# Performance work log

Hardware: AMD Instinct MI355X
Metric: run time of the kernel (lower is better)

## Reference

```python
import jax, jax.numpy as jnp
import numpy as np

SEQ, B, IN, H = 512, 64, 1024, 1024

def _lstm_layer(x_seq, Wx, bx, Wh, bh):
    # x_seq: [S, B, D], Wx: [4H, D], Wh: [4H, H]
    h0 = jnp.zeros((x_seq.shape[1], Wh.shape[1]), x_seq.dtype)
    c0 = jnp.zeros_like(h0)
    def step(carry, x_t):
        h, c = carry
        z = x_t @ Wx.T + bx + h @ Wh.T + bh  # [B, 4H]
        i, f, g, o = jnp.split(z, 4, axis=1)
        c1 = jax.nn.sigmoid(f) * c + jax.nn.sigmoid(i) * jnp.tanh(g)
        h1 = jax.nn.sigmoid(o) * jnp.tanh(c1)
        return (h1, c1), h1
    _, hs = jax.lax.scan(step, (h0, c0), x_seq)
    return hs  # [S, B, H]

def setup_inputs() -> dict:
    key = jax.random.key(0)
    ks = jax.random.split(key, 9)
    s_in = 1.0 / np.sqrt(IN)
    s_h = 1.0 / np.sqrt(H)
    return {
        "x": jax.random.normal(ks[0], (SEQ, B, IN), jnp.float32),
        "Wx0": jax.random.uniform(ks[1], (4 * H, IN), jnp.float32, -s_in, s_in),
        "bx0": jax.random.uniform(ks[2], (4 * H,), jnp.float32, -s_in, s_in),
        "Wh0": jax.random.uniform(ks[3], (4 * H, H), jnp.float32, -s_h, s_h),
        "bh0": jax.random.uniform(ks[4], (4 * H,), jnp.float32, -s_h, s_h),
        "Wx1": jax.random.uniform(ks[5], (4 * H, H), jnp.float32, -s_h, s_h),
        "bx1": jax.random.uniform(ks[6], (4 * H,), jnp.float32, -s_h, s_h),
        "Wh1": jax.random.uniform(ks[7], (4 * H, H), jnp.float32, -s_h, s_h),
        "bh1": jax.random.uniform(ks[8], (4 * H,), jnp.float32, -s_h, s_h),
    }

def reference(x, Wx0, bx0, Wh0, bh0, Wx1, bx1, Wh1, bh1):
    # Two stacked unidirectional LSTM layers, zero initial states.
    h_seq0 = _lstm_layer(x, Wx0, bx0, Wh0, bh0)
    h_seq1 = _lstm_layer(h_seq0, Wx1, bx1, Wh1, bh1)
    return h_seq1  # [S, B, H] = stacked version of the torch list output
```

## Files before the change

kernel.cpp:

```cpp
#include <hip/hip_runtime.h>


#define SEQ   512
#define BATCH 64
#define HID   1024
#define NG    4096
#define KCAT  2048
#define EPOCH_IDX 8192

typedef __attribute__((ext_vector_type(8))) _Float16 f16x8;
typedef __attribute__((ext_vector_type(4))) _Float16 f16x4;
typedef __attribute__((ext_vector_type(4))) float    f32x4;

__device__ __forceinline__ float sigm_f(float x){ return 1.f/(1.f + __expf(-x)); }
__device__ __forceinline__ float tanh_f(float x){
    float e = __expf(-2.f*fabsf(x));
    float r = (1.f - e)/(1.f + e);
    return copysignf(r, x);
}

__device__ __forceinline__ void store_h8(_Float16* p, f16x4 v){
    asm volatile("global_store_dwordx2 %0, %1, off sc0 sc1" :: "v"(p), "v"(v) : "memory");
}
__device__ __forceinline__ void drain_vmem(){
    asm volatile("s_waitcnt vmcnt(0)" ::: "memory");
}


__global__ void prep_w_kernel(const float* __restrict__ Wx, const float* __restrict__ Wh,
                              const float* __restrict__ bx, const float* __restrict__ bh,
                              _Float16* __restrict__ Wr, float* __restrict__ br){
    int p = blockIdx.x;
    int j = p >> 2, g = p & 3;
    int r = g*1024 + j;
    int k = threadIdx.x * 8;
    const float* s = (k < 1024) ? (Wx + (size_t)r*1024 + k)
                                : (Wh + (size_t)r*1024 + (k - 1024));
    float4 v0 = *reinterpret_cast<const float4*>(s);
    float4 v1 = *reinterpret_cast<const float4*>(s + 4);
    f16x8 o;
    o[0]=(_Float16)v0.x; o[1]=(_Float16)v0.y; o[2]=(_Float16)v0.z; o[3]=(_Float16)v0.w;
    o[4]=(_Float16)v1.x; o[5]=(_Float16)v1.y; o[6]=(_Float16)v1.z; o[7]=(_Float16)v1.w;
    *reinterpret_cast<f16x8*>(Wr + (size_t)p*KCAT + k) = o;
    if (threadIdx.x == 0) br[p] = bx[r] + bh[r];
}

__global__ void prep_x_kernel(const float* __restrict__ x, _Float16* xo){
    size_t i = ((size_t)blockIdx.x*256 + threadIdx.x) * 8;
    float4 v0 = *reinterpret_cast<const float4*>(x + i);
    float4 v1 = *reinterpret_cast<const float4*>(x + i + 4);
    f16x8 o;
    o[0]=(_Float16)v0.x; o[1]=(_Float16)v0.y; o[2]=(_Float16)v0.z; o[3]=(_Float16)v0.w;
    o[4]=(_Float16)v1.x; o[5]=(_Float16)v1.y; o[6]=(_Float16)v1.z; o[7]=(_Float16)v1.w;
    *reinterpret_cast<f16x8*>(xo + i) = o;
}

__global__ void init_misc_kernel(int* flags, _Float16* hz){
    int i = blockIdx.x*256 + threadIdx.x;
    flags[i] = 0;
    size_t j = (size_t)i * 4;
    if (j < (size_t)BATCH*HID){
        f16x4 z; z[0]=(_Float16)0.f; z[1]=(_Float16)0.f; z[2]=(_Float16)0.f; z[3]=(_Float16)0.f;
        *reinterpret_cast<f16x4*>(hz + j) = z;
    }
}


__device__ __forceinline__ void wait_epoch_g(const int* flags, int k, int rep){
    for(;;){
        int e = __hip_atomic_load(&flags[EPOCH_IDX + rep*32], __ATOMIC_RELAXED, __HIP_MEMORY_SCOPE_AGENT);
        if (e >= k) break;
        __builtin_amdgcn_s_sleep(2);
    }
    asm volatile("" ::: "memory");
}

__device__ __forceinline__ void aggregate_publish(int* flags, int k, int lane){
    const int b = lane*4;
    for(;;){
        int a0 = __hip_atomic_load(&flags[(b+0)*32], __ATOMIC_RELAXED, __HIP_MEMORY_SCOPE_AGENT);
        int a1 = __hip_atomic_load(&flags[(b+1)*32], __ATOMIC_RELAXED, __HIP_MEMORY_SCOPE_AGENT);
        int a2 = __hip_atomic_load(&flags[(b+2)*32], __ATOMIC_RELAXED, __HIP_MEMORY_SCOPE_AGENT);
        int a3 = __hip_atomic_load(&flags[(b+3)*32], __ATOMIC_RELAXED, __HIP_MEMORY_SCOPE_AGENT);
        bool ok = (a0>=k) && (a1>=k) && (a2>=k) && (a3>=k);
        if (__all(ok)) break;
        __builtin_amdgcn_s_sleep(1);
    }
    asm volatile("" ::: "memory");
    if (lane < 8)
        __hip_atomic_store(&flags[EPOCH_IDX + lane*32], k, __ATOMIC_RELAXED, __HIP_MEMORY_SCOPE_AGENT);
}

__device__ __forceinline__ void lds_publish(int* e, int k){
    __hip_atomic_store(e, k, __ATOMIC_RELAXED, __HIP_MEMORY_SCOPE_WORKGROUP);
}
__device__ __forceinline__ void lds_wait(int* e, int k){
    while (__hip_atomic_load(e, __ATOMIC_RELAXED, __HIP_MEMORY_SCOPE_WORKGROUP) < k)
        __builtin_amdgcn_s_sleep(1);
    asm volatile("" ::: "memory");
}


__device__ __forceinline__ f32x4 mfma16(f16x8 a, f16x8 b, f32x4 c){
    return __builtin_amdgcn_mfma_f32_16x16x32_f16(a, b, c, 0, 0, 0);
}

__device__ __forceinline__ void gemm_q_f16(const _Float16* A, const _Float16* Wp, f32x4* acc){
    #pragma unroll 4
    for (int kk = 0; kk < 16; ++kk){
        f16x8 b  = *reinterpret_cast<const f16x8*>(Wp + kk*32);
        f16x8 a0 = *reinterpret_cast<const f16x8*>(A + kk*32);
        f16x8 a1 = *reinterpret_cast<const f16x8*>(A + kk*32 + 16*1024);
        f16x8 a2 = *reinterpret_cast<const f16x8*>(A + kk*32 + 32*1024);
        f16x8 a3 = *reinterpret_cast<const f16x8*>(A + kk*32 + 48*1024);
        acc[0] = mfma16(a0, b, acc[0]);
        acc[1] = mfma16(a1, b, acc[1]);
        acc[2] = mfma16(a2, b, acc[2]);
        acc[3] = mfma16(a3, b, acc[3]);
    }
}

__device__ __forceinline__ void gemm_q_f32(const float* A, const _Float16* Wp, f32x4* acc){
    #pragma unroll 2
    for (int kk = 0; kk < 16; ++kk){
        f16x8 b = *reinterpret_cast<const f16x8*>(Wp + kk*32);
        f16x8 a[4];
        #pragma unroll
        for (int m = 0; m < 4; ++m){
            float4 u0 = *reinterpret_cast<const float4*>(A + kk*32 + (size_t)m*16*1024);
            float4 u1 = *reinterpret_cast<const float4*>(A + kk*32 + (size_t)m*16*1024 + 4);
            f16x8 v;
            v[0]=(_Float16)u0.x; v[1]=(_Float16)u0.y; v[2]=(_Float16)u0.z; v[3]=(_Float16)u0.w;
            v[4]=(_Float16)u1.x; v[5]=(_Float16)u1.y; v[6]=(_Float16)u1.z; v[7]=(_Float16)u1.w;
            a[m] = v;
        }
        acc[0] = mfma16(a[0], b, acc[0]);
        acc[1] = mfma16(a[1], b, acc[1]);
        acc[2] = mfma16(a[2], b, acc[2]);
        acc[3] = mfma16(a[3], b, acc[3]);
    }
}


__global__ __launch_bounds__(256, 1)
void lstm_persist(const _Float16* __restrict__ Wr0, const _Float16* __restrict__ Wr1,
                  const float* __restrict__ br0, const float* __restrict__ br1,
                  const _Float16* __restrict__ xbf, const float* __restrict__ xf32,
                  int use_xf16, const _Float16* __restrict__ hz,
                  _Float16* h0ring, _Float16* h1ring, float* out, int* flags){
    const int tid  = threadIdx.x;
    const int wg   = blockIdx.x;
    const int wv   = tid >> 6;
    const int lane = tid & 63;
    const int r    = lane & 15;
    const int q    = lane >> 4;
    const int p0   = wg * 16;
    const int rep  = wg & 7;

    __shared__ float accL[2][4][64][17];
    __shared__ int   lds_epoch;

    if (tid == 0) lds_epoch = 0;
    __syncthreads();

    f32x4 cst = {0.f,0.f,0.f,0.f};
    f32x4 ho_keep = {0.f,0.f,0.f,0.f};
    f32x4 bias[4];
    {
        const float* bsrc = (wv == 0) ? br0 : br1;
        #pragma unroll
        for (int jj = 0; jj < 4; ++jj)
            bias[jj] = *reinterpret_cast<const f32x4*>(&bsrc[p0 + jj*4]);
    }

    const int kofs = (wv & 1)*512 + q*8;
    const int wcol = wv*512 + q*8;

    for (int k = 0; k <= SEQ; ++k){
        f32x4 acc0[4], acc1[4];
        #pragma unroll
        for (int m = 0; m < 4; ++m){
            acc0[m].x=0;acc0[m].y=0;acc0[m].z=0;acc0[m].w=0;
            acc1[m].x=0;acc1[m].y=0;acc1[m].z=0;acc1[m].w=0;
        }

        if (wv < 2){
            if (k < SEQ){
                if (use_xf16)
                    gemm_q_f16(xbf + (size_t)k*BATCH*HID + (size_t)r*HID + kofs,
                               Wr0 + (size_t)(p0 + r)*KCAT + wcol, acc0);
                else
                    gemm_q_f32(xf32 + (size_t)k*BATCH*1024 + (size_t)r*1024 + kofs,
                               Wr0 + (size_t)(p0 + r)*KCAT + wcol, acc0);
            }
            if (k > 0){
                lds_wait(&lds_epoch, k);
                gemm_q_f16(h0ring + (size_t)(k-1)*BATCH*HID + (size_t)r*HID + kofs,
                           Wr1 + (size_t)(p0 + r)*KCAT + wcol, acc1);
            }
        } else {
            if (k > 0){
                if (wv == 3){
                    if (wg == 0) aggregate_publish(flags, k, lane);
                    else         wait_epoch_g(flags, k, rep);
                    lds_publish(&lds_epoch, k);
                } else {
                    lds_wait(&lds_epoch, k);
                }
            }
            if (k < SEQ){
                const _Float16* A0 = (k == 0) ? (hz + (size_t)r*HID + kofs)
                                              : (h0ring + (size_t)(k-1)*BATCH*HID + (size_t)r*HID + kofs);
                gemm_q_f16(A0, Wr0 + (size_t)(p0 + r)*KCAT + wcol, acc0);
            }
            if (k >= 1){
                const _Float16* A1 = (k == 1) ? (hz + (size_t)r*HID + kofs)
                                              : (h1ring + (size_t)(k-2)*BATCH*HID + (size_t)r*HID + kofs);
                gemm_q_f16(A1, Wr1 + (size_t)(p0 + r)*KCAT + wcol, acc1);
            }
        }

        __syncthreads();

        #pragma unroll
        for (int mt = 0; mt < 4; ++mt){
            #pragma unroll
            for (int j = 0; j < 4; ++j){
                accL[0][wv][mt*16 + q*4 + j][r] = acc0[mt][j];
                accL[1][wv][mt*16 + q*4 + j][r] = acc1[mt][j];
            }
        }
        __syncthreads();

        if (wv == 0 && k < SEQ){
            f32x4 zz[4];
            #pragma unroll
            for (int jj = 0; jj < 4; ++jj) zz[jj] = bias[jj];
            #pragma unroll
            for (int w2 = 0; w2 < 4; ++w2)
                #pragma unroll
                for (int jj = 0; jj < 4; ++jj){
                    f32x4 a = *reinterpret_cast<const f32x4*>(&accL[0][w2][lane][jj*4]);
                    zz[jj].x += a.x; zz[jj].y += a.y; zz[jj].z += a.z; zz[jj].w += a.w;
                }
            f16x4 hv;
            #pragma unroll
            for (int jl = 0; jl < 4; ++jl){
                float ig = sigm_f(zz[jl].x), fg = sigm_f(zz[jl].y);
                float gg = tanh_f(zz[jl].z), og = sigm_f(zz[jl].w);
                float c = fg*cst[jl] + ig*gg;  cst[jl] = c;
                hv[jl] = (_Float16)(og * tanh_f(c));
            }
            store_h8(h0ring + ((size_t)k*BATCH + lane)*HID + wg*4, hv);
            drain_vmem();
        }
        if (wv == 1 && k >= 1){
            const int t1 = k - 1;
            f32x4 zz[4];
            #pragma unroll
            for (int jj = 0; jj < 4; ++jj) zz[jj] = bias[jj];
            #pragma unroll
            for (int w2 = 0; w2 < 4; ++w2)
                #pragma unroll
                for (int jj = 0; jj < 4; ++jj){
                    f32x4 a = *reinterpret_cast<const f32x4*>(&accL[1][w2][lane][jj*4]);
                    zz[jj].x += a.x; zz[jj].y += a.y; zz[jj].z += a.z; zz[jj].w += a.w;
                }
            f16x4 hv; f32x4 ho;
            #pragma unroll
            for (int jl = 0; jl < 4; ++jl){
                float ig = sigm_f(zz[jl].x), fg = sigm_f(zz[jl].y);
                float gg = tanh_f(zz[jl].z), og = sigm_f(zz[jl].w);
                float c = fg*cst[jl] + ig*gg;  cst[jl] = c;
                float h = og * tanh_f(c);
                hv[jl] = (_Float16)h;  ho[jl] = h;
            }
            if (k < SEQ) store_h8(h1ring + ((size_t)t1*BATCH + lane)*HID + wg*4, hv);
            if (t1 < SEQ-1) *reinterpret_cast<f32x4*>(out + ((size_t)t1*BATCH + lane)*HID + wg*4) = ho;
            else            ho_keep = ho;
            drain_vmem();
        }

        __syncthreads();
        if (tid == 0)
            __hip_atomic_store(&flags[wg*32], k + 1, __ATOMIC_RELAXED, __HIP_MEMORY_SCOPE_AGENT);
    }

    if (wv == 3){
        if (wg == 0) aggregate_publish(flags, SEQ + 1, lane);
        else         wait_epoch_g(flags, SEQ + 1, rep);
        lds_publish(&lds_epoch, SEQ + 1);
    }
    if (wv == 1){
        lds_wait(&lds_epoch, SEQ + 1);
        *reinterpret_cast<f32x4*>(out + ((size_t)(SEQ-1)*BATCH + lane)*HID + wg*4) = ho_keep;
    }
}


extern "C" void kernel_launch(void* const* d_in, const int* in_sizes, int n_in,
                              void* d_out, int out_size, void* d_ws, size_t ws_size,
                              hipStream_t stream){
    const float* x   = (const float*)d_in[0];
    const float* Wx0 = (const float*)d_in[1];
    const float* bx0 = (const float*)d_in[2];
    const float* Wh0 = (const float*)d_in[3];
    const float* bh0 = (const float*)d_in[4];
    const float* Wx1 = (const float*)d_in[5];
    const float* bx1 = (const float*)d_in[6];
    const float* Wh1 = (const float*)d_in[7];
    const float* bh1 = (const float*)d_in[8];
    float* out = (float*)d_out;
    char* ws = (char*)d_ws;

    size_t o = 0;
    _Float16* Wr0 = (_Float16*)(ws + o); o += (size_t)NG*KCAT*2;
    _Float16* Wr1 = (_Float16*)(ws + o); o += (size_t)NG*KCAT*2;
    float* br0 = (float*)(ws + o); o += 16384;
    float* br1 = (float*)(ws + o); o += 16384;
    _Float16* h1ring = (_Float16*)(ws + o); o += (size_t)SEQ*BATCH*HID*2;
    _Float16* hz     = (_Float16*)(ws + o); o += (size_t)BATCH*HID*2;
    int* flags = (int*)(ws + o); o += 65536;

    const size_t RING = (size_t)SEQ*BATCH*HID*2;
    _Float16 *xbf = nullptr, *h0ring;
    int use_xf16 = 0;
    if (ws_size >= o + 2*RING){
        xbf    = (_Float16*)(ws + o);  o += RING;  use_xf16 = 1;
        h0ring = (_Float16*)(ws + o);  o += RING;
    } else if (ws_size >= o + RING){
        xbf    = (_Float16*)(ws + o);  o += RING;  use_xf16 = 1;
        h0ring = (_Float16*)((char*)d_out + (size_t)64*1024*1024);
    } else {
        h0ring = (_Float16*)((char*)d_out + (size_t)64*1024*1024);
    }

    prep_w_kernel<<<NG, 256, 0, stream>>>(Wx0, Wh0, bx0, bh0, Wr0, br0);
    prep_w_kernel<<<NG, 256, 0, stream>>>(Wx1, Wh1, bx1, bh1, Wr1, br1);
    if (use_xf16)
        prep_x_kernel<<<(SEQ*BATCH*HID)/(256*8), 256, 0, stream>>>(x, xbf);
    init_misc_kernel<<<64, 256, 0, stream>>>(flags, hz);
    lstm_persist<<<256, 256, 0, stream>>>(Wr0, Wr1, br0, br1, xbf, x, use_xf16,
                                          hz, h0ring, h1ring, out, flags);
}
```

Before: 10.89 ms.

## Keep recurrent weight slices resident in swizzled LDS for the persistent kernel

Each persistent workgroup now copies its 16-row slices of the recurrent weights (Wh0 and the full Wx1/Wh1 row) into dynamic shared memory once, using an XOR swizzle against bank conflicts. The per-step GEMMs on the serial path then read B operands from LDS instead of global/L2 on every timestep. This raises LDS usage to about 130KB per block and requires the max dynamic shared memory attribute. The non-recurrent x-projection still streams weights from global.

```diff
diff --git a/kernel.cpp b/kernel.cpp
--- a/kernel.cpp
+++ b/kernel.cpp
@@ -7,6 +7,8 @@
 #define NG    4096
 #define KCAT  2048
 #define EPOCH_IDX 8192
+
+#define SMEM_BYTES 133504
 
 typedef __attribute__((ext_vector_type(8))) _Float16 f16x8;
 typedef __attribute__((ext_vector_type(4))) _Float16 f16x4;
@@ -141,6 +143,22 @@
     }
 }
 
+__device__ __forceinline__ void gemm_q_ldsb(const _Float16* A, const char* wrow,
+                                            int c0, int swz, f32x4* acc){
+    #pragma unroll 4
+    for (int kk = 0; kk < 16; ++kk){
+        f16x8 b  = *reinterpret_cast<const f16x8*>(wrow + ((c0 + kk*64) ^ swz));
+        f16x8 a0 = *reinterpret_cast<const f16x8*>(A + kk*32);
+        f16x8 a1 = *reinterpret_cast<const f16x8*>(A + kk*32 + 16*1024);
+        f16x8 a2 = *reinterpret_cast<const f16x8*>(A + kk*32 + 32*1024);
+        f16x8 a3 = *reinterpret_cast<const f16x8*>(A + kk*32 + 48*1024);
+        acc[0] = mfma16(a0, b, acc[0]);
+        acc[1] = mfma16(a1, b, acc[1]);
+        acc[2] = mfma16(a2, b, acc[2]);
+        acc[3] = mfma16(a3, b, acc[3]);
+    }
+}
+
 
 __global__ __launch_bounds__(256, 1)
 void lstm_persist(const _Float16* __restrict__ Wr0, const _Float16* __restrict__ Wr1,
@@ -148,6 +166,10 @@
                   const _Float16* __restrict__ xbf, const float* __restrict__ xf32,
                   int use_xf16, const _Float16* __restrict__ hz,
                   _Float16* h0ring, _Float16* h1ring, float* out, int* flags){
+    extern __shared__ char smem[];
+    float (*accL)[4][64][17] = reinterpret_cast<float(*)[4][64][17]>(smem + 98304);
+    int* lds_epoch = reinterpret_cast<int*>(smem + 133120);
+
     const int tid  = threadIdx.x;
     const int wg   = blockIdx.x;
     const int wv   = tid >> 6;
@@ -156,11 +178,23 @@
     const int q    = lane >> 4;
     const int p0   = wg * 16;
     const int rep  = wg & 7;
-
-    __shared__ float accL[2][4][64][17];
-    __shared__ int   lds_epoch;
-
-    if (tid == 0) lds_epoch = 0;
+    const int swz  = (r & 7) << 4;
+
+    for (int idx = tid; idx < 6144; idx += 256){
+        int rr, cb; char* dst; const _Float16* s;
+        if (idx < 2048){
+            rr = idx >> 7;  cb = (idx & 127) << 4;
+            s   = Wr0 + (size_t)(p0 + rr)*KCAT + 1024 + (cb >> 1);
+            dst = smem + rr*2048 + (cb ^ ((rr & 7) << 4));
+        } else {
+            int j2 = idx - 2048;
+            rr = j2 >> 8;  cb = (j2 & 255) << 4;
+            s   = Wr1 + (size_t)(p0 + rr)*KCAT + (cb >> 1);
+            dst = smem + 32768 + rr*4096 + (cb ^ ((rr & 7) << 4));
+        }
+        *reinterpret_cast<f16x8*>(dst) = *reinterpret_cast<const f16x8*>(s);
+    }
+    if (tid == 0) *lds_epoch = 0;
     __syncthreads();
 
     f32x4 cst = {0.f,0.f,0.f,0.f};
@@ -175,6 +209,8 @@
 
     const int kofs = (wv & 1)*512 + q*8;
     const int wcol = wv*512 + q*8;
+    const char* w1row  = smem + 32768 + r*4096;
+    const char* wh0row = smem + r*2048;
 
     for (int k = 0; k <= SEQ; ++k){
         f32x4 acc0[4], acc1[4];
@@ -194,29 +230,29 @@
                                Wr0 + (size_t)(p0 + r)*KCAT + wcol, acc0);
             }
             if (k > 0){
-                lds_wait(&lds_epoch, k);
-                gemm_q_f16(h0ring + (size_t)(k-1)*BATCH*HID + (size_t)r*HID + kofs,
-                           Wr1 + (size_t)(p0 + r)*KCAT + wcol, acc1);
+                lds_wait(lds_epoch, k);
+                gemm_q_ldsb(h0ring + (size_t)(k-1)*BATCH*HID + (size_t)r*HID + kofs,
+                            w1row, wv*1024 + q*16, swz, acc1);
             }
         } else {
             if (k > 0){
                 if (wv == 3){
                     if (wg == 0) aggregate_publish(flags, k, lane);
                     else         wait_epoch_g(flags, k, rep);
-                    lds_publish(&lds_epoch, k);
+                    lds_publish(lds_epoch, k);
                 } else {
-                    lds_wait(&lds_epoch, k);
+                    lds_wait(lds_epoch, k);
                 }
             }
             if (k < SEQ){
                 const _Float16* A0 = (k == 0) ? (hz + (size_t)r*HID + kofs)
                                               : (h0ring + (size_t)(k-1)*BATCH*HID + (size_t)r*HID + kofs);
-                gemm_q_f16(A0, Wr0 + (size_t)(p0 + r)*KCAT + wcol, acc0);
+                gemm_q_ldsb(A0, wh0row, (wv-2)*1024 + q*16, swz, acc0);
             }
             if (k >= 1){
                 const _Float16* A1 = (k == 1) ? (hz + (size_t)r*HID + kofs)
                                               : (h1ring + (size_t)(k-2)*BATCH*HID + (size_t)r*HID + kofs);
-                gemm_q_f16(A1, Wr1 + (size_t)(p0 + r)*KCAT + wcol, acc1);
+                gemm_q_ldsb(A1, w1row, wv*1024 + q*16, swz, acc1);
             }
         }
 
@@ -289,10 +325,10 @@
     if (wv == 3){
         if (wg == 0) aggregate_publish(flags, SEQ + 1, lane);
         else         wait_epoch_g(flags, SEQ + 1, rep);
-        lds_publish(&lds_epoch, SEQ + 1);
+        lds_publish(lds_epoch, SEQ + 1);
     }
     if (wv == 1){
-        lds_wait(&lds_epoch, SEQ + 1);
+        lds_wait(lds_epoch, SEQ + 1);
         *reinterpret_cast<f32x4*>(out + ((size_t)(SEQ-1)*BATCH + lane)*HID + wg*4) = ho_keep;
     }
 }
@@ -335,11 +371,14 @@
         h0ring = (_Float16*)((char*)d_out + (size_t)64*1024*1024);
     }
 
+    hipFuncSetAttribute((const void*)lstm_persist,
+                        hipFuncAttributeMaxDynamicSharedMemorySize, SMEM_BYTES);
+
     prep_w_kernel<<<NG, 256, 0, stream>>>(Wx0, Wh0, bx0, bh0, Wr0, br0);
     prep_w_kernel<<<NG, 256, 0, stream>>>(Wx1, Wh1, bx1, bh1, Wr1, br1);
     if (use_xf16)
         prep_x_kernel<<<(SEQ*BATCH*HID)/(256*8), 256, 0, stream>>>(x, xbf);
     init_misc_kernel<<<64, 256, 0, stream>>>(flags, hz);
-    lstm_persist<<<256, 256, 0, stream>>>(Wr0, Wr1, br0, br1, xbf, x, use_xf16,
-                                          hz, h0ring, h1ring, out, flags);
-}
+    lstm_persist<<<256, 256, SMEM_BYTES, stream>>>(Wr0, Wr1, br0, br1, xbf, x, use_xf16,
+                                                   hz, h0ring, h1ring, out, flags);
+}
```

Result: faster. 9.838 ms (-9.7%).
